# Kernel optimization log

Measured on AMD Instinct MI355X. Metric: run time of the kernel, lower is better.

Reference implementation:

```python
import jax, jax.numpy as jnp
import numpy as np

N_NODES = 100000
N_EDGES = 640000
NODE_D = 128   # node_emb_dim == edge_type_emb_dim (required by reverse-net input dim)
MSG_D = 128


def setup_inputs() -> dict:
    key = jax.random.key(0)
    ks = jax.random.split(key, 10)
    cat_d = 3 * NODE_D  # 2*node_emb + edge_type_emb
    s_msg = 1.0 / np.sqrt(cat_d)
    s_upd = 1.0 / np.sqrt(MSG_D)
    return {
        "node_features": jax.random.normal(ks[0], (N_NODES, NODE_D), jnp.float32),
        "edge_features": jax.random.normal(ks[1], (N_EDGES, NODE_D), jnp.float32),
        "from_idx": jax.random.randint(ks[2], (N_EDGES,), 0, N_NODES, jnp.int32),
        "to_idx": jax.random.randint(ks[3], (N_EDGES,), 0, N_NODES, jnp.int32),
        # message net (Linear + ReLU)
        "W_msg": jax.random.uniform(ks[4], (cat_d, MSG_D), jnp.float32, -s_msg, s_msg),
        "b_msg": jnp.zeros((MSG_D,), jnp.float32),
        # reverse message net (separate params)
        "W_rev": jax.random.uniform(ks[5], (cat_d, MSG_D), jnp.float32, -s_msg, s_msg),
        "b_rev": jnp.zeros((MSG_D,), jnp.float32),
        # node-update MLP (Linear + ReLU), residual update
        "W_upd": jax.random.uniform(ks[6], (MSG_D, NODE_D), jnp.float32, -s_upd, s_upd),
        "b_upd": jnp.zeros((NODE_D,), jnp.float32),
    }


def reference(node_features, edge_features, from_idx, to_idx,
              W_msg, b_msg, W_rev, b_rev, W_upd, b_upd):
    # gather endpoints and concat with edge features: [n_edges, 3*node_d]
    edge_inputs = jnp.concatenate(
        [node_features[from_idx], node_features[to_idx], edge_features], axis=-1)
    # forward + reverse message nets (same inputs, different params), summed
    messages = (jax.nn.relu(edge_inputs @ W_msg + b_msg)
                + jax.nn.relu(edge_inputs @ W_rev + b_rev))
    # scatter-sum into destination nodes: [n_nodes, msg_d]
    aggregated = jax.ops.segment_sum(messages, to_idx, num_segments=N_NODES)
    # residual node update: node + MLP(agg)
    return node_features + jax.nn.relu(aggregated @ W_upd + b_upd)
```

## Files before the change

kernel.cpp:

```cpp
#include <hip/hip_runtime.h>
#include <hip/hip_bf16.h>

#define N_NODES 100000
#define N_EDGES 640000

typedef __bf16 bf16_t;
typedef __bf16 bf16x8 __attribute__((ext_vector_type(8)));
typedef float f32x4 __attribute__((ext_vector_type(4)));
typedef float f4 __attribute__((ext_vector_type(4)));
typedef unsigned int u32x4 __attribute__((ext_vector_type(4)));

__device__ __forceinline__ float bflo(unsigned int u) { return __uint_as_float(u << 16); }
__device__ __forceinline__ float bfhi(unsigned int u) { return __uint_as_float(u & 0xffff0000u); }
__device__ __forceinline__ unsigned int bfpack(float a, float b) {
    union { bf16_t h[2]; unsigned int u; } pk;
    pk.h[0] = (bf16_t)a; pk.h[1] = (bf16_t)b;
    return pk.u;
}

__global__ void hist_kernel(const int* __restrict__ to_idx, int* __restrict__ hist) {
    int e = blockIdx.x * 256 + threadIdx.x;
    if (e < N_EDGES) atomicAdd(&hist[to_idx[e]], 1);
}

#define SCAN_CH 1000

__global__ __launch_bounds__(1024)
void scan_reduce_kernel(const int* __restrict__ hist, int* __restrict__ bsum) {
    __shared__ int red[1024];
    int b = blockIdx.x, t = threadIdx.x;
    int v = (t < SCAN_CH) ? hist[b * SCAN_CH + t] : 0;
    red[t] = v;
    __syncthreads();
    for (int off = 512; off > 0; off >>= 1) {
        if (t < off) red[t] += red[t + off];
        __syncthreads();
    }
    if (t == 0) bsum[b] = red[0];
}

__global__ __launch_bounds__(128)
void scan_base_kernel(const int* __restrict__ bsum, int* __restrict__ bbase) {
    __shared__ int s[128];
    int t = threadIdx.x;
    int v = (t < 100) ? bsum[t] : 0;
    s[t] = v;
    __syncthreads();
    for (int off = 1; off < 128; off <<= 1) {
        int u = (t >= off) ? s[t - off] : 0;
        __syncthreads();
        s[t] += u;
        __syncthreads();
    }
    if (t < 100) bbase[t] = s[t] - v;
}

__global__ __launch_bounds__(1024)
void scan_final_kernel(const int* __restrict__ hist,
                       const int* __restrict__ bbase,
                       int* __restrict__ cursor,
                       int* __restrict__ row_start) {
    __shared__ int s[1024];
    int b = blockIdx.x, t = threadIdx.x;
    int v = (t < SCAN_CH) ? hist[b * SCAN_CH + t] : 0;
    s[t] = v;
    __syncthreads();
    for (int off = 1; off < 1024; off <<= 1) {
        int u = (t >= off) ? s[t - off] : 0;
        __syncthreads();
        s[t] += u;
        __syncthreads();
    }
    int excl = bbase[b] + s[t] - v;
    if (t < SCAN_CH) {
        cursor[b * SCAN_CH + t] = excl;
        row_start[b * SCAN_CH + t] = excl;
    }
    if (b == 99 && t == SCAN_CH - 1) row_start[N_NODES] = excl + v;
}

__global__ void inv_scatter_kernel(const int* __restrict__ to_idx,
                                   int* __restrict__ cursor,
                                   int* __restrict__ inv) {
    int e = blockIdx.x * 256 + threadIdx.x;
    if (e < N_EDGES) {
        int pos = atomicAdd(&cursor[to_idx[e]], 1);
        inv[e] = pos;
    }
}

__global__ void prep_w_new(const float* __restrict__ Wmsg,
                           const float* __restrict__ Wrev,
                           const float* __restrict__ Wupd,
                           bf16_t* __restrict__ Wt1,
                           bf16_t* __restrict__ WtE,
                           bf16_t* __restrict__ WtU) {
    int idx = blockIdx.x * 256 + threadIdx.x;
    if (idx < 512 * 128) {
        int p = idx >> 7, k = idx & 127;
        int blk = p >> 7, c = p & 127;
        float v;
        if (blk == 0)      v = Wmsg[k * 128 + c];
        else if (blk == 1) v = Wrev[k * 128 + c];
        else if (blk == 2) v = Wmsg[(128 + k) * 128 + c];
        else               v = Wrev[(128 + k) * 128 + c];
        Wt1[idx] = (bf16_t)v;
    }
    if (idx < 256 * 128) {
        int p = idx >> 7, k = idx & 127;
        float v = (p < 128) ? Wmsg[(256 + k) * 128 + p]
                            : Wrev[(256 + k) * 128 + (p - 128)];
        WtE[idx] = (bf16_t)v;
    }
    if (idx < 128 * 128) {
        int n = idx >> 7, p = idx & 127;
        int colp = 32 * (p >> 5) + ((p >> 1) & 15) + 16 * (p & 1);
        WtU[idx] = (bf16_t)Wupd[colp * 128 + n];
    }
}

__global__ __launch_bounds__(512, 4)
void proj_node_kernel(const float* __restrict__ nodef,
                      const bf16_t* __restrict__ Wt1,
                      unsigned int* __restrict__ A_u) {
    __shared__ char lds_raw[64 * 256];
    const int tid = threadIdx.x;
    const int nb = blockIdx.x * 64;
    const int by = blockIdx.y;

#pragma unroll
    for (int j = 0; j < 4; ++j) {
        int linear = tid + 512 * j;
        int r = linear >> 5, q = linear & 31;
        int node = nb + r;
        f4 v = (f4){0.f, 0.f, 0.f, 0.f};
        if (node < N_NODES)
            v = *reinterpret_cast<const f4*>(nodef + (size_t)node * 128 + q * 4);
        union { bf16_t b[4]; uint2 u; } pk;
        pk.b[0] = (bf16_t)v[0]; pk.b[1] = (bf16_t)v[1];
        pk.b[2] = (bf16_t)v[2]; pk.b[3] = (bf16_t)v[3];
        int byte = (r * 256 + q * 8) ^ ((r & 7) << 4);
        *reinterpret_cast<uint2*>(lds_raw + byte) = pk.u;
    }
    __syncthreads();

    const int wv = tid >> 6;
    const int wr = wv >> 2, wc = wv & 3;
    const int lane = tid & 63;
    const int lhi = lane >> 4, llo = lane & 15;

    f32x4 acc[2][4];
#pragma unroll
    for (int m = 0; m < 2; ++m)
#pragma unroll
        for (int n = 0; n < 4; ++n)
            acc[m][n] = (f32x4){0.f, 0.f, 0.f, 0.f};

    const bf16_t* bptr[4];
#pragma unroll
    for (int n = 0; n < 4; ++n) {
        int colb = (n < 2) ? (wc * 32 + 16 * n) : (128 + wc * 32 + 16 * (n - 2));
        bptr[n] = Wt1 + (size_t)(by * 256 + colb + llo) * 128 + lhi * 8;
    }

#pragma unroll
    for (int k0 = 0; k0 < 4; ++k0) {
        bf16x8 a[2], b[4];
#pragma unroll
        for (int m = 0; m < 2; ++m) {
            int ra = wr * 32 + 16 * m + llo;
            int byte = (ra * 256 + (k0 * 32 + lhi * 8) * 2) ^ ((ra & 7) << 4);
            a[m] = *reinterpret_cast<const bf16x8*>(lds_raw + byte);
        }
#pragma unroll
        for (int n = 0; n < 4; ++n)
            b[n] = *reinterpret_cast<const bf16x8*>(bptr[n] + k0 * 32);
#pragma unroll
        for (int m = 0; m < 2; ++m)
#pragma unroll
            for (int n = 0; n < 4; ++n)
                acc[m][n] = __builtin_amdgcn_mfma_f32_16x16x32_bf16(a[m], b[n], acc[m][n], 0, 0, 0);
    }

    const int wli = wc * 16 + llo;
#pragma unroll
    for (int m = 0; m < 2; ++m) {
        int rbase = wr * 32 + 16 * m + lhi * 4;
#pragma unroll
        for (int r = 0; r < 4; ++r) {
            int node = nb + rbase + r;
            if (node < N_NODES) {
                size_t base = (size_t)node * 256 + by * 128;
                uint2 pr;
                pr.x = bfpack(acc[m][0][r], acc[m][1][r]);
                pr.y = bfpack(acc[m][2][r], acc[m][3][r]);
                *reinterpret_cast<uint2*>(A_u + base + 2 * wli) = pr;
            }
        }
    }
}

__global__ __launch_bounds__(256, 4)
void edge_fused_kernel(const float* __restrict__ edgef,
                       const int* __restrict__ from_idx,
                       const int* __restrict__ to_idx,
                       const int* __restrict__ inv,
                       const unsigned int* __restrict__ A_u,
                       const bf16_t* __restrict__ WtE,
                       const float* __restrict__ b_msg,
                       const float* __restrict__ b_rev,
                       unsigned int* __restrict__ msgs_u) {
    __shared__ char lds_raw[32 * 256];
    __shared__ int s_from[32], s_dst[32], s_inv[32];

    const int tid = threadIdx.x;
    const int eb = blockIdx.x * 32;

    if (tid < 32) {
        s_from[tid] = from_idx[eb + tid];
        s_dst[tid]  = to_idx[eb + tid];
        s_inv[tid]  = inv[eb + tid];
    }

#pragma unroll
    for (int j = 0; j < 4; ++j) {
        int linear = tid + 256 * j;
        int r = linear >> 5, q = linear & 31;
        f4 v = *reinterpret_cast<const f4*>(edgef + (size_t)(eb + r) * 128 + q * 4);
        union { bf16_t b[4]; uint2 u; } pk;
        pk.b[0] = (bf16_t)v[0]; pk.b[1] = (bf16_t)v[1];
        pk.b[2] = (bf16_t)v[2]; pk.b[3] = (bf16_t)v[3];
        int byte = (r * 256 + q * 8) ^ ((r & 7) << 4);
        *reinterpret_cast<uint2*>(lds_raw + byte) = pk.u;
    }
    __syncthreads();

    const int wc = tid >> 6;
    const int lane = tid & 63;
    const int lhi = lane >> 4, llo = lane & 15;
    const int wli = wc * 16 + llo;

    uint2 gF[2][4], gT[2][4];
#pragma unroll
    for (int m = 0; m < 2; ++m) {
#pragma unroll
        for (int r = 0; r < 4; ++r) {
            int rr = 16 * m + lhi * 4 + r;
            gF[m][r] = *reinterpret_cast<const uint2*>(
                A_u + (size_t)s_from[rr] * 256 + 2 * wli);
            gT[m][r] = *reinterpret_cast<const uint2*>(
                A_u + (size_t)s_dst[rr] * 256 + 128 + 2 * wli);
        }
    }

    f32x4 acc[2][4];
#pragma unroll
    for (int m = 0; m < 2; ++m)
#pragma unroll
        for (int n = 0; n < 4; ++n)
            acc[m][n] = (f32x4){0.f, 0.f, 0.f, 0.f};

    const bf16_t* bptr[4];
#pragma unroll
    for (int n = 0; n < 4; ++n) {
        int colb = (n < 2) ? (wc * 32 + 16 * n) : (128 + wc * 32 + 16 * (n - 2));
        bptr[n] = WtE + (size_t)(colb + llo) * 128 + lhi * 8;
    }

#pragma unroll
    for (int k0 = 0; k0 < 4; ++k0) {
        bf16x8 a[2], b[4];
#pragma unroll
        for (int m = 0; m < 2; ++m) {
            int ra = 16 * m + llo;
            int byte = (ra * 256 + (k0 * 32 + lhi * 8) * 2) ^ ((ra & 7) << 4);
            a[m] = *reinterpret_cast<const bf16x8*>(lds_raw + byte);
        }
#pragma unroll
        for (int n = 0; n < 4; ++n)
            b[n] = *reinterpret_cast<const bf16x8*>(bptr[n] + k0 * 32);
#pragma unroll
        for (int m = 0; m < 2; ++m)
#pragma unroll
            for (int n = 0; n < 4; ++n)
                acc[m][n] = __builtin_amdgcn_mfma_f32_16x16x32_bf16(a[m], b[n], acc[m][n], 0, 0, 0);
    }

    const int c0 = wc * 32 + llo;
    const float bm0 = b_msg[c0], bm1 = b_msg[c0 + 16];
    const float br0 = b_rev[c0], br1 = b_rev[c0 + 16];
#pragma unroll
    for (int m = 0; m < 2; ++m) {
#pragma unroll
        for (int r = 0; r < 4; ++r) {
            int rr = 16 * m + lhi * 4 + r;
            float m0 = fmaxf(acc[m][0][r] + bm0 + bflo(gF[m][r].x) + bflo(gT[m][r].x), 0.f);
            float m1 = fmaxf(acc[m][1][r] + bm1 + bfhi(gF[m][r].x) + bfhi(gT[m][r].x), 0.f);
            float r0 = fmaxf(acc[m][2][r] + br0 + bflo(gF[m][r].y) + bflo(gT[m][r].y), 0.f);
            float r1 = fmaxf(acc[m][3][r] + br1 + bfhi(gF[m][r].y) + bfhi(gT[m][r].y), 0.f);
            msgs_u[(size_t)s_inv[rr] * 64 + wli] = bfpack(m0 + r0, m1 + r1);
        }
    }
}

__global__ __launch_bounds__(256, 4)
void node_upd_kernel(const unsigned int* __restrict__ msgs_u,
                     const int* __restrict__ row_start,
                     const float* __restrict__ nodef,
                     const bf16_t* __restrict__ WtU,
                     const float* __restrict__ b_upd,
                     float* __restrict__ out) {
    __shared__ char lds_raw[64 * 256];
    __shared__ int s_rs[65];

    const int tid = threadIdx.x;
    const int nb = blockIdx.x * 64;

    if (tid < 65) {
        int nid = nb + tid;
        s_rs[tid] = (nid <= N_NODES) ? row_start[nid] : N_EDGES;
    }
    __syncthreads();

    {
        const int r = tid >> 2;
        const int q = tid & 3;
        float s[32];
#pragma unroll
        for (int i = 0; i < 32; ++i) s[i] = 0.f;
        const int rs = s_rs[r], re = s_rs[r + 1];
        int e = rs;
        for (; e + 1 < re; e += 2) {
            const u32x4* p0 = reinterpret_cast<const u32x4*>(msgs_u + (size_t)e * 64 + q * 16);
            const u32x4* p1 = reinterpret_cast<const u32x4*>(msgs_u + (size_t)(e + 1) * 64 + q * 16);
            u32x4 w0[4], w1[4];
#pragma unroll
            for (int i = 0; i < 4; ++i) { w0[i] = p0[i]; w1[i] = p1[i]; }
#pragma unroll
            for (int i = 0; i < 4; ++i) {
                s[8*i+0] += bflo(w0[i][0]) + bflo(w1[i][0]);
                s[8*i+1] += bfhi(w0[i][0]) + bfhi(w1[i][0]);
                s[8*i+2] += bflo(w0[i][1]) + bflo(w1[i][1]);
                s[8*i+3] += bfhi(w0[i][1]) + bfhi(w1[i][1]);
                s[8*i+4] += bflo(w0[i][2]) + bflo(w1[i][2]);
                s[8*i+5] += bfhi(w0[i][2]) + bfhi(w1[i][2]);
                s[8*i+6] += bflo(w0[i][3]) + bflo(w1[i][3]);
                s[8*i+7] += bfhi(w0[i][3]) + bfhi(w1[i][3]);
            }
        }
        if (e < re) {
            const u32x4* p = reinterpret_cast<const u32x4*>(msgs_u + (size_t)e * 64 + q * 16);
#pragma unroll
            for (int i = 0; i < 4; ++i) {
                u32x4 w = p[i];
                s[8*i+0] += bflo(w[0]); s[8*i+1] += bfhi(w[0]);
                s[8*i+2] += bflo(w[1]); s[8*i+3] += bfhi(w[1]);
                s[8*i+4] += bflo(w[2]); s[8*i+5] += bfhi(w[2]);
                s[8*i+6] += bflo(w[3]); s[8*i+7] += bfhi(w[3]);
            }
        }
#pragma unroll
        for (int i = 0; i < 4; ++i) {
            union { bf16_t b[8]; u32x4 u; } pk;
#pragma unroll
            for (int w = 0; w < 8; ++w) pk.b[w] = (bf16_t)s[8*i + w];
            int byte = (r * 256 + q * 64 + i * 16) ^ ((r & 7) << 4);
            *reinterpret_cast<u32x4*>(lds_raw + byte) = pk.u;
        }
    }
    __syncthreads();

    const int wv = tid >> 6;
    const int lane = tid & 63;
    const int lhi = lane >> 4, llo = lane & 15;

    f32x4 acc[4][2];
#pragma unroll
    for (int m = 0; m < 4; ++m)
#pragma unroll
        for (int n = 0; n < 2; ++n)
            acc[m][n] = (f32x4){0.f, 0.f, 0.f, 0.f};

#pragma unroll
    for (int k0 = 0; k0 < 4; ++k0) {
        bf16x8 a[4], b[2];
#pragma unroll
        for (int m = 0; m < 4; ++m) {
            int ra = 16 * m + llo;
            int byte = (ra * 256 + (k0 * 32 + lhi * 8) * 2) ^ ((ra & 7) << 4);
            a[m] = *reinterpret_cast<const bf16x8*>(lds_raw + byte);
        }
#pragma unroll
        for (int n = 0; n < 2; ++n) {
            int col = wv * 32 + 16 * n + llo;
            b[n] = *reinterpret_cast<const bf16x8*>(WtU + (size_t)col * 128 + k0 * 32 + lhi * 8);
        }
#pragma unroll
        for (int m = 0; m < 4; ++m)
#pragma unroll
            for (int n = 0; n < 2; ++n)
                acc[m][n] = __builtin_amdgcn_mfma_f32_16x16x32_bf16(a[m], b[n], acc[m][n], 0, 0, 0);
    }

#pragma unroll
    for (int m = 0; m < 4; ++m) {
        int rbase = 16 * m + lhi * 4;
#pragma unroll
        for (int r = 0; r < 4; ++r) {
            int i = nb + rbase + r;
            if (i < N_NODES) {
#pragma unroll
                for (int n = 0; n < 2; ++n) {
                    int c = wv * 32 + 16 * n + llo;
                    out[(size_t)i * 128 + c] =
                        nodef[(size_t)i * 128 + c]
                        + fmaxf(acc[m][n][r] + b_upd[c], 0.f);
                }
            }
        }
    }
}

__global__ __launch_bounds__(256)
void convert_nodef_kernel(const float* __restrict__ nodef,
                          unsigned short* __restrict__ nodef_bf) {
    int i = blockIdx.x * 256 + threadIdx.x;
    if (i < N_NODES * 32) {
        f4 v = *reinterpret_cast<const f4*>(nodef + (size_t)i * 4);
        union { bf16_t b[4]; unsigned long long ll; } pk;
        pk.b[0] = (bf16_t)v[0]; pk.b[1] = (bf16_t)v[1];
        pk.b[2] = (bf16_t)v[2]; pk.b[3] = (bf16_t)v[3];
        *reinterpret_cast<unsigned long long*>(nodef_bf + (size_t)i * 4) = pk.ll;
    }
}

__global__ void prep_w_old(const float* __restrict__ Wmsg,
                           const float* __restrict__ Wrev,
                           const float* __restrict__ Wupd,
                           bf16_t* __restrict__ WtAB,
                           bf16_t* __restrict__ WtU) {
    int idx = blockIdx.x * 256 + threadIdx.x;
    if (idx < 256 * 384) {
        int n = idx / 384;
        int k = idx - n * 384;
        float v = (n < 128) ? Wmsg[k * 128 + n] : Wrev[k * 128 + (n - 128)];
        WtAB[idx] = (bf16_t)v;
    }
    if (idx < 128 * 128) {
        int n = idx >> 7, p = idx & 127;
        int colp = 32 * (p >> 5) + ((p >> 1) & 15) + 16 * (p & 1);
        WtU[idx] = (bf16_t)Wupd[colp * 128 + n];
    }
}

__global__ __launch_bounds__(512, 4)
void edge_msg_old_kernel(const unsigned short* __restrict__ nodef_bf,
                         const float* __restrict__ edgef,
                         const int* __restrict__ from_idx,
                         const int* __restrict__ to_idx,
                         const int* __restrict__ inv,
                         const bf16_t* __restrict__ WtAB,
                         const float* __restrict__ b_msg,
                         const float* __restrict__ b_rev,
                         unsigned int* __restrict__ msgs_u) {
    __shared__ char lds_raw[64 * 384];
    __shared__ int s_from[64], s_dst[64], s_inv[64];

    const int tid = threadIdx.x;
    const int eb = blockIdx.x * 64;

    if (tid < 64) {
        s_from[tid] = from_idx[eb + tid];
        s_dst[tid]  = to_idx[eb + tid];
        s_inv[tid]  = inv[eb + tid];
    }

    const int wv = tid >> 6;
    const int wr = wv >> 2, wc = wv & 3;
    const int lane = tid & 63;
    const int lhi = lane >> 4, llo = lane & 15;

    f32x4 acc[2][4];
#pragma unroll
    for (int m = 0; m < 2; ++m)
#pragma unroll
        for (int n = 0; n < 4; ++n)
            acc[m][n] = (f32x4){0.f, 0.f, 0.f, 0.f};

    const bf16_t* bptr[4];
#pragma unroll
    for (int n = 0; n < 4; ++n) {
        int colb = (n < 2) ? (wc * 32 + 16 * n) : (128 + wc * 32 + 16 * (n - 2));
        bptr[n] = WtAB + (size_t)(colb + llo) * 384 + lhi * 8;
    }

    __syncthreads();

#pragma unroll
    for (int j = 0; j < 3; ++j) {
        int linear = tid + 512 * j;
        int r = linear / 24;
        int q = linear - r * 24;
        const u32x4* src = (q < 16)
            ? reinterpret_cast<const u32x4*>(nodef_bf + (size_t)s_from[r] * 128) + q
            : reinterpret_cast<const u32x4*>(nodef_bf + (size_t)s_dst[r] * 128) + (q - 16);
        u32x4 v = *src;
        int byte = (r * 384 + q * 16) ^ ((r & 7) << 4);
        *reinterpret_cast<u32x4*>(lds_raw + byte) = v;
    }
    __syncthreads();

#pragma unroll
    for (int k0 = 0; k0 < 6; ++k0) {
        bf16x8 a[2], b[4];
#pragma unroll
        for (int m = 0; m < 2; ++m) {
            int ra = wr * 32 + 16 * m + llo;
            int byte = (ra * 384 + k0 * 64 + lhi * 16) ^ ((ra & 7) << 4);
            a[m] = *reinterpret_cast<const bf16x8*>(lds_raw + byte);
        }
#pragma unroll
        for (int n = 0; n < 4; ++n)
            b[n] = *reinterpret_cast<const bf16x8*>(bptr[n] + k0 * 32);
#pragma unroll
        for (int m = 0; m < 2; ++m)
#pragma unroll
            for (int n = 0; n < 4; ++n)
                acc[m][n] = __builtin_amdgcn_mfma_f32_16x16x32_bf16(a[m], b[n], acc[m][n], 0, 0, 0);
    }
    __syncthreads();

#pragma unroll
    for (int j = 0; j < 3; ++j) {
        int linear = tid + 512 * j;
        int r = linear / 24;
        int qq = linear - r * 24;
        u32x4 w;
        if (qq < 8) {
            w = *(reinterpret_cast<const u32x4*>(nodef_bf + (size_t)s_dst[r] * 128) + 8 + qq);
        } else {
            int c = qq - 8;
            const f4* ep = reinterpret_cast<const f4*>(edgef + (size_t)(eb + r) * 128 + c * 8);
            f4 v0 = ep[0];
            f4 v1 = ep[1];
            union { bf16_t b[8]; u32x4 u; } pk;
            pk.b[0] = (bf16_t)v0[0]; pk.b[1] = (bf16_t)v0[1];
            pk.b[2] = (bf16_t)v0[2]; pk.b[3] = (bf16_t)v0[3];
            pk.b[4] = (bf16_t)v1[0]; pk.b[5] = (bf16_t)v1[1];
            pk.b[6] = (bf16_t)v1[2]; pk.b[7] = (bf16_t)v1[3];
            w = pk.u;
        }
        int byte = (r * 384 + qq * 16) ^ ((r & 7) << 4);
        *reinterpret_cast<u32x4*>(lds_raw + byte) = w;
    }
    __syncthreads();

#pragma unroll
    for (int k0 = 0; k0 < 6; ++k0) {
        bf16x8 a[2], b[4];
#pragma unroll
        for (int m = 0; m < 2; ++m) {
            int ra = wr * 32 + 16 * m + llo;
            int byte = (ra * 384 + k0 * 64 + lhi * 16) ^ ((ra & 7) << 4);
            a[m] = *reinterpret_cast<const bf16x8*>(lds_raw + byte);
        }
#pragma unroll
        for (int n = 0; n < 4; ++n)
            b[n] = *reinterpret_cast<const bf16x8*>(bptr[n] + (6 + k0) * 32);
#pragma unroll
        for (int m = 0; m < 2; ++m)
#pragma unroll
            for (int n = 0; n < 4; ++n)
                acc[m][n] = __builtin_amdgcn_mfma_f32_16x16x32_bf16(a[m], b[n], acc[m][n], 0, 0, 0);
    }

    const int c0 = wc * 32 + llo;
    const float bm0 = b_msg[c0], br0 = b_rev[c0];
    const float bm1 = b_msg[c0 + 16], br1 = b_rev[c0 + 16];
#pragma unroll
    for (int m = 0; m < 2; ++m) {
        int rbase = wr * 32 + 16 * m + lhi * 4;
#pragma unroll
        for (int r = 0; r < 4; ++r) {
            float v0 = fmaxf(acc[m][0][r] + bm0, 0.f) + fmaxf(acc[m][2][r] + br0, 0.f);
            float v1 = fmaxf(acc[m][1][r] + bm1, 0.f) + fmaxf(acc[m][3][r] + br1, 0.f);
            msgs_u[(size_t)s_inv[rbase + r] * 64 + wc * 16 + llo] = bfpack(v0, v1);
        }
    }
}

extern "C" void kernel_launch(void* const* d_in, const int* in_sizes, int n_in,
                              void* d_out, int out_size, void* d_ws, size_t ws_size,
                              hipStream_t stream) {
    const float* nodef    = (const float*)d_in[0];
    const float* edgef    = (const float*)d_in[1];
    const int*   from_idx = (const int*)d_in[2];
    const int*   to_idx   = (const int*)d_in[3];
    const float* Wmsg     = (const float*)d_in[4];
    const float* bmsg     = (const float*)d_in[5];
    const float* Wrev     = (const float*)d_in[6];
    const float* brev     = (const float*)d_in[7];
    const float* Wupd     = (const float*)d_in[8];
    const float* bupd     = (const float*)d_in[9];
    float* out = (float*)d_out;
    char* ws = (char*)d_ws;

    if (ws_size >= 271000000) {
        unsigned int* A_u      = (unsigned int*)ws;
        unsigned int* msgs_u   = (unsigned int*)(ws + 102400000);
        bf16_t*       Wt1      = (bf16_t*)(ws + 266240000);
        bf16_t*       WtE      = (bf16_t*)(ws + 266371072);
        bf16_t*       WtU      = (bf16_t*)(ws + 266436608);
        int*          hist     = (int*)(ws + 266469376);
        int*          cursor   = (int*)(ws + 266869376);
        int*          rowstart = (int*)(ws + 267269376);
        int*          inv      = (int*)(ws + 267669392);
        int*          bsum     = (int*)(ws + 270229392);
        int*          bbase    = (int*)(ws + 270229792);

        hipMemsetAsync(hist, 0, (size_t)N_NODES * sizeof(int), stream);
        prep_w_new<<<256, 256, 0, stream>>>(Wmsg, Wrev, Wupd, Wt1, WtE, WtU);
        hist_kernel<<<(N_EDGES + 255) / 256, 256, 0, stream>>>(to_idx, hist);
        scan_reduce_kernel<<<100, 1024, 0, stream>>>(hist, bsum);
        scan_base_kernel<<<1, 128, 0, stream>>>(bsum, bbase);
        scan_final_kernel<<<100, 1024, 0, stream>>>(hist, bbase, cursor, rowstart);
        inv_scatter_kernel<<<(N_EDGES + 255) / 256, 256, 0, stream>>>(to_idx, cursor, inv);
        proj_node_kernel<<<dim3((N_NODES + 63) / 64, 2), 512, 0, stream>>>(nodef, Wt1, A_u);
        edge_fused_kernel<<<N_EDGES / 32, 256, 0, stream>>>(
            edgef, from_idx, to_idx, inv, A_u, WtE, bmsg, brev, msgs_u);
        node_upd_kernel<<<(N_NODES + 63) / 64, 256, 0, stream>>>(
            msgs_u, rowstart, nodef, WtU, bupd, out);
    } else {
        unsigned int*   msgs_u   = (unsigned int*)ws;
        bf16_t*         WtAB     = (bf16_t*)(ws + 163840000);
        bf16_t*         WtU      = (bf16_t*)(ws + 164036608);
        unsigned short* nodef_bf = (unsigned short*)(ws + 164069376);
        int*            hist     = (int*)(ws + 189669376);
        int*            cursor   = (int*)(ws + 190069376);
        int*            rowstart = (int*)(ws + 190469376);
        int*            inv      = (int*)(ws + 190869392);
        int*            bsum     = (int*)(ws + 193429392);
        int*            bbase    = (int*)(ws + 193429792);

        hipMemsetAsync(hist, 0, (size_t)N_NODES * sizeof(int), stream);
        convert_nodef_kernel<<<12500, 256, 0, stream>>>(nodef, nodef_bf);
        prep_w_old<<<384, 256, 0, stream>>>(Wmsg, Wrev, Wupd, WtAB, WtU);
        hist_kernel<<<(N_EDGES + 255) / 256, 256, 0, stream>>>(to_idx, hist);
        scan_reduce_kernel<<<100, 1024, 0, stream>>>(hist, bsum);
        scan_base_kernel<<<1, 128, 0, stream>>>(bsum, bbase);
        scan_final_kernel<<<100, 1024, 0, stream>>>(hist, bbase, cursor, rowstart);
        inv_scatter_kernel<<<(N_EDGES + 255) / 256, 256, 0, stream>>>(to_idx, cursor, inv);
        edge_msg_old_kernel<<<N_EDGES / 64, 512, 0, stream>>>(
            nodef_bf, edgef, from_idx, to_idx, inv, WtAB, bmsg, brev, msgs_u);
        node_upd_kernel<<<(N_NODES + 63) / 64, 256, 0, stream>>>(
            msgs_u, rowstart, nodef, WtU, bupd, out);
    }
}
```

Baseline: 457.8 us.

## Process four edge tiles per block with double-buffered LDS staging in edge kernel

The edge kernel now handles 128 edges per block as four 32-edge tiles. Each tile's edge features are prefetched into registers and written to a second LDS buffer while the current tile's MFMAs run, so global loads overlap compute. The launch count drops by a factor of four, which also amortises the per-block index and bias setup. The small-workspace fallback path and its old kernels are removed, so the code now assumes a large enough workspace, and the extra live registers may reduce occupancy.

```diff
diff --git a/kernel.cpp b/kernel.cpp
--- a/kernel.cpp
+++ b/kernel.cpp
@@ -210,56 +210,23 @@
                        const float* __restrict__ b_msg,
                        const float* __restrict__ b_rev,
                        unsigned int* __restrict__ msgs_u) {
-    __shared__ char lds_raw[32 * 256];
-    __shared__ int s_from[32], s_dst[32], s_inv[32];
+    __shared__ char lds_raw[2][8192];
+    __shared__ int s_from[128], s_dst[128], s_inv[128];
 
     const int tid = threadIdx.x;
-    const int eb = blockIdx.x * 32;
-
-    if (tid < 32) {
-        s_from[tid] = from_idx[eb + tid];
-        s_dst[tid]  = to_idx[eb + tid];
-        s_inv[tid]  = inv[eb + tid];
-    }
-
-#pragma unroll
-    for (int j = 0; j < 4; ++j) {
-        int linear = tid + 256 * j;
-        int r = linear >> 5, q = linear & 31;
-        f4 v = *reinterpret_cast<const f4*>(edgef + (size_t)(eb + r) * 128 + q * 4);
-        union { bf16_t b[4]; uint2 u; } pk;
-        pk.b[0] = (bf16_t)v[0]; pk.b[1] = (bf16_t)v[1];
-        pk.b[2] = (bf16_t)v[2]; pk.b[3] = (bf16_t)v[3];
-        int byte = (r * 256 + q * 8) ^ ((r & 7) << 4);
-        *reinterpret_cast<uint2*>(lds_raw + byte) = pk.u;
-    }
-    __syncthreads();
+    const size_t eb0 = (size_t)blockIdx.x * 128;
+
+    if (tid < 128) {
+        s_from[tid] = from_idx[eb0 + tid];
+        s_dst[tid]  = to_idx[eb0 + tid];
+        s_inv[tid]  = inv[eb0 + tid];
+    }
 
     const int wc = tid >> 6;
     const int lane = tid & 63;
     const int lhi = lane >> 4, llo = lane & 15;
     const int wli = wc * 16 + llo;
 
-    uint2 gF[2][4], gT[2][4];
-#pragma unroll
-    for (int m = 0; m < 2; ++m) {
-#pragma unroll
-        for (int r = 0; r < 4; ++r) {
-            int rr = 16 * m + lhi * 4 + r;
-            gF[m][r] = *reinterpret_cast<const uint2*>(
-                A_u + (size_t)s_from[rr] * 256 + 2 * wli);
-            gT[m][r] = *reinterpret_cast<const uint2*>(
-                A_u + (size_t)s_dst[rr] * 256 + 128 + 2 * wli);
-        }
-    }
-
-    f32x4 acc[2][4];
-#pragma unroll
-    for (int m = 0; m < 2; ++m)
-#pragma unroll
-        for (int n = 0; n < 4; ++n)
-            acc[m][n] = (f32x4){0.f, 0.f, 0.f, 0.f};
-
     const bf16_t* bptr[4];
 #pragma unroll
     for (int n = 0; n < 4; ++n) {
@@ -267,39 +234,128 @@
         bptr[n] = WtE + (size_t)(colb + llo) * 128 + lhi * 8;
     }
 
-#pragma unroll
-    for (int k0 = 0; k0 < 4; ++k0) {
-        bf16x8 a[2], b[4];
-#pragma unroll
-        for (int m = 0; m < 2; ++m) {
-            int ra = 16 * m + llo;
-            int byte = (ra * 256 + (k0 * 32 + lhi * 8) * 2) ^ ((ra & 7) << 4);
-            a[m] = *reinterpret_cast<const bf16x8*>(lds_raw + byte);
-        }
-#pragma unroll
-        for (int n = 0; n < 4; ++n)
-            b[n] = *reinterpret_cast<const bf16x8*>(bptr[n] + k0 * 32);
-#pragma unroll
-        for (int m = 0; m < 2; ++m)
-#pragma unroll
-            for (int n = 0; n < 4; ++n)
-                acc[m][n] = __builtin_amdgcn_mfma_f32_16x16x32_bf16(a[m], b[n], acc[m][n], 0, 0, 0);
-    }
-
     const int c0 = wc * 32 + llo;
     const float bm0 = b_msg[c0], bm1 = b_msg[c0 + 16];
     const float br0 = b_rev[c0], br1 = b_rev[c0 + 16];
-#pragma unroll
-    for (int m = 0; m < 2; ++m) {
-#pragma unroll
-        for (int r = 0; r < 4; ++r) {
-            int rr = 16 * m + lhi * 4 + r;
-            float m0 = fmaxf(acc[m][0][r] + bm0 + bflo(gF[m][r].x) + bflo(gT[m][r].x), 0.f);
-            float m1 = fmaxf(acc[m][1][r] + bm1 + bfhi(gF[m][r].x) + bfhi(gT[m][r].x), 0.f);
-            float r0 = fmaxf(acc[m][2][r] + br0 + bflo(gF[m][r].y) + bflo(gT[m][r].y), 0.f);
-            float r1 = fmaxf(acc[m][3][r] + br1 + bfhi(gF[m][r].y) + bfhi(gT[m][r].y), 0.f);
-            msgs_u[(size_t)s_inv[rr] * 64 + wli] = bfpack(m0 + r0, m1 + r1);
-        }
+
+    f4 st[4];
+#pragma unroll
+    for (int j = 0; j < 4; ++j) {
+        int lin = tid + 256 * j, r = lin >> 5, q = lin & 31;
+        st[j] = *reinterpret_cast<const f4*>(edgef + (eb0 + r) * 128 + q * 4);
+    }
+#pragma unroll
+    for (int j = 0; j < 4; ++j) {
+        int lin = tid + 256 * j, r = lin >> 5, q = lin & 31;
+        union { bf16_t b[4]; uint2 u; } pk;
+        pk.b[0] = (bf16_t)st[j][0]; pk.b[1] = (bf16_t)st[j][1];
+        pk.b[2] = (bf16_t)st[j][2]; pk.b[3] = (bf16_t)st[j][3];
+        int byte = (r * 256 + q * 8) ^ ((r & 7) << 4);
+        *reinterpret_cast<uint2*>(&lds_raw[0][0] + byte) = pk.u;
+    }
+    __syncthreads();
+
+#pragma unroll
+    for (int t = 0; t < 4; ++t) {
+        const int cur = t & 1;
+
+        bf16x8 bA[2][4];
+#pragma unroll
+        for (int k0 = 0; k0 < 2; ++k0)
+#pragma unroll
+            for (int n = 0; n < 4; ++n)
+                bA[k0][n] = *reinterpret_cast<const bf16x8*>(bptr[n] + k0 * 32);
+
+        uint2 gF[2][4], gT[2][4];
+#pragma unroll
+        for (int m = 0; m < 2; ++m)
+#pragma unroll
+            for (int r = 0; r < 4; ++r) {
+                int rr = t * 32 + 16 * m + lhi * 4 + r;
+                gF[m][r] = *reinterpret_cast<const uint2*>(
+                    A_u + (size_t)s_from[rr] * 256 + 2 * wli);
+                gT[m][r] = *reinterpret_cast<const uint2*>(
+                    A_u + (size_t)s_dst[rr] * 256 + 128 + 2 * wli);
+            }
+
+        if (t < 3) {
+#pragma unroll
+            for (int j = 0; j < 4; ++j) {
+                int lin = tid + 256 * j, r = lin >> 5, q = lin & 31;
+                st[j] = *reinterpret_cast<const f4*>(
+                    edgef + (eb0 + (size_t)(t + 1) * 32 + r) * 128 + q * 4);
+            }
+        }
+
+        f32x4 acc[2][4];
+#pragma unroll
+        for (int m = 0; m < 2; ++m)
+#pragma unroll
+            for (int n = 0; n < 4; ++n)
+                acc[m][n] = (f32x4){0.f, 0.f, 0.f, 0.f};
+#pragma unroll
+        for (int k0 = 0; k0 < 2; ++k0) {
+            bf16x8 a[2];
+#pragma unroll
+            for (int m = 0; m < 2; ++m) {
+                int ra = 16 * m + llo;
+                int byte = (ra * 256 + (k0 * 32 + lhi * 8) * 2) ^ ((ra & 7) << 4);
+                a[m] = *reinterpret_cast<const bf16x8*>(&lds_raw[cur][0] + byte);
+            }
+#pragma unroll
+            for (int m = 0; m < 2; ++m)
+#pragma unroll
+                for (int n = 0; n < 4; ++n)
+                    acc[m][n] = __builtin_amdgcn_mfma_f32_16x16x32_bf16(a[m], bA[k0][n], acc[m][n], 0, 0, 0);
+        }
+
+#pragma unroll
+        for (int k0 = 0; k0 < 2; ++k0)
+#pragma unroll
+            for (int n = 0; n < 4; ++n)
+                bA[k0][n] = *reinterpret_cast<const bf16x8*>(bptr[n] + (2 + k0) * 32);
+
+#pragma unroll
+        for (int k0 = 0; k0 < 2; ++k0) {
+            bf16x8 a[2];
+#pragma unroll
+            for (int m = 0; m < 2; ++m) {
+                int ra = 16 * m + llo;
+                int byte = (ra * 256 + ((2 + k0) * 32 + lhi * 8) * 2) ^ ((ra & 7) << 4);
+                a[m] = *reinterpret_cast<const bf16x8*>(&lds_raw[cur][0] + byte);
+            }
+#pragma unroll
+            for (int m = 0; m < 2; ++m)
+#pragma unroll
+                for (int n = 0; n < 4; ++n)
+                    acc[m][n] = __builtin_amdgcn_mfma_f32_16x16x32_bf16(a[m], bA[k0][n], acc[m][n], 0, 0, 0);
+        }
+
+        if (t < 3) {
+#pragma unroll
+            for (int j = 0; j < 4; ++j) {
+                int lin = tid + 256 * j, r = lin >> 5, q = lin & 31;
+                union { bf16_t b[4]; uint2 u; } pk;
+                pk.b[0] = (bf16_t)st[j][0]; pk.b[1] = (bf16_t)st[j][1];
+                pk.b[2] = (bf16_t)st[j][2]; pk.b[3] = (bf16_t)st[j][3];
+                int byte = (r * 256 + q * 8) ^ ((r & 7) << 4);
+                *reinterpret_cast<uint2*>(&lds_raw[cur ^ 1][0] + byte) = pk.u;
+            }
+        }
+
+#pragma unroll
+        for (int m = 0; m < 2; ++m)
+#pragma unroll
+            for (int r = 0; r < 4; ++r) {
+                int rr = t * 32 + 16 * m + lhi * 4 + r;
+                float m0 = fmaxf(acc[m][0][r] + bm0 + bflo(gF[m][r].x) + bflo(gT[m][r].x), 0.f);
+                float m1 = fmaxf(acc[m][1][r] + bm1 + bfhi(gF[m][r].x) + bfhi(gT[m][r].x), 0.f);
+                float r0 = fmaxf(acc[m][2][r] + br0 + bflo(gF[m][r].y) + bflo(gT[m][r].y), 0.f);
+                float r1 = fmaxf(acc[m][3][r] + br1 + bfhi(gF[m][r].y) + bfhi(gT[m][r].y), 0.f);
+                msgs_u[(size_t)s_inv[rr] * 64 + wli] = bfpack(m0 + r0, m1 + r1);
+            }
+
+        __syncthreads();
     }
 }
 
@@ -417,174 +473,6 @@
                         + fmaxf(acc[m][n][r] + b_upd[c], 0.f);
                 }
             }
-        }
-    }
-}
-
-__global__ __launch_bounds__(256)
-void convert_nodef_kernel(const float* __restrict__ nodef,
-                          unsigned short* __restrict__ nodef_bf) {
-    int i = blockIdx.x * 256 + threadIdx.x;
-    if (i < N_NODES * 32) {
-        f4 v = *reinterpret_cast<const f4*>(nodef + (size_t)i * 4);
-        union { bf16_t b[4]; unsigned long long ll; } pk;
-        pk.b[0] = (bf16_t)v[0]; pk.b[1] = (bf16_t)v[1];
-        pk.b[2] = (bf16_t)v[2]; pk.b[3] = (bf16_t)v[3];
-        *reinterpret_cast<unsigned long long*>(nodef_bf + (size_t)i * 4) = pk.ll;
-    }
-}
-
-__global__ void prep_w_old(const float* __restrict__ Wmsg,
-                           const float* __restrict__ Wrev,
-                           const float* __restrict__ Wupd,
-                           bf16_t* __restrict__ WtAB,
-                           bf16_t* __restrict__ WtU) {
-    int idx = blockIdx.x * 256 + threadIdx.x;
-    if (idx < 256 * 384) {
-        int n = idx / 384;
-        int k = idx - n * 384;
-        float v = (n < 128) ? Wmsg[k * 128 + n] : Wrev[k * 128 + (n - 128)];
-        WtAB[idx] = (bf16_t)v;
-    }
-    if (idx < 128 * 128) {
-        int n = idx >> 7, p = idx & 127;
-        int colp = 32 * (p >> 5) + ((p >> 1) & 15) + 16 * (p & 1);
-        WtU[idx] = (bf16_t)Wupd[colp * 128 + n];
-    }
-}
-
-__global__ __launch_bounds__(512, 4)
-void edge_msg_old_kernel(const unsigned short* __restrict__ nodef_bf,
-                         const float* __restrict__ edgef,
-                         const int* __restrict__ from_idx,
-                         const int* __restrict__ to_idx,
-                         const int* __restrict__ inv,
-                         const bf16_t* __restrict__ WtAB,
-                         const float* __restrict__ b_msg,
-                         const float* __restrict__ b_rev,
-                         unsigned int* __restrict__ msgs_u) {
-    __shared__ char lds_raw[64 * 384];
-    __shared__ int s_from[64], s_dst[64], s_inv[64];
-
-    const int tid = threadIdx.x;
-    const int eb = blockIdx.x * 64;
-
-    if (tid < 64) {
-        s_from[tid] = from_idx[eb + tid];
-        s_dst[tid]  = to_idx[eb + tid];
-        s_inv[tid]  = inv[eb + tid];
-    }
-
-    const int wv = tid >> 6;
-    const int wr = wv >> 2, wc = wv & 3;
-    const int lane = tid & 63;
-    const int lhi = lane >> 4, llo = lane & 15;
-
-    f32x4 acc[2][4];
-#pragma unroll
-    for (int m = 0; m < 2; ++m)
-#pragma unroll
-        for (int n = 0; n < 4; ++n)
-            acc[m][n] = (f32x4){0.f, 0.f, 0.f, 0.f};
-
-    const bf16_t* bptr[4];
-#pragma unroll
-    for (int n = 0; n < 4; ++n) {
-        int colb = (n < 2) ? (wc * 32 + 16 * n) : (128 + wc * 32 + 16 * (n - 2));
-        bptr[n] = WtAB + (size_t)(colb + llo) * 384 + lhi * 8;
-    }
-
-    __syncthreads();
-
-#pragma unroll
-    for (int j = 0; j < 3; ++j) {
-        int linear = tid + 512 * j;
-        int r = linear / 24;
-        int q = linear - r * 24;
-        const u32x4* src = (q < 16)
-            ? reinterpret_cast<const u32x4*>(nodef_bf + (size_t)s_from[r] * 128) + q
-            : reinterpret_cast<const u32x4*>(nodef_bf + (size_t)s_dst[r] * 128) + (q - 16);
-        u32x4 v = *src;
-        int byte = (r * 384 + q * 16) ^ ((r & 7) << 4);
-        *reinterpret_cast<u32x4*>(lds_raw + byte) = v;
-    }
-    __syncthreads();
-
-#pragma unroll
-    for (int k0 = 0; k0 < 6; ++k0) {
-        bf16x8 a[2], b[4];
-#pragma unroll
-        for (int m = 0; m < 2; ++m) {
-            int ra = wr * 32 + 16 * m + llo;
-            int byte = (ra * 384 + k0 * 64 + lhi * 16) ^ ((ra & 7) << 4);
-            a[m] = *reinterpret_cast<const bf16x8*>(lds_raw + byte);
-        }
-#pragma unroll
-        for (int n = 0; n < 4; ++n)
-            b[n] = *reinterpret_cast<const bf16x8*>(bptr[n] + k0 * 32);
-#pragma unroll
-        for (int m = 0; m < 2; ++m)
-#pragma unroll
-            for (int n = 0; n < 4; ++n)
-                acc[m][n] = __builtin_amdgcn_mfma_f32_16x16x32_bf16(a[m], b[n], acc[m][n], 0, 0, 0);
-    }
-    __syncthreads();
-
-#pragma unroll
-    for (int j = 0; j < 3; ++j) {
-        int linear = tid + 512 * j;
-        int r = linear / 24;
-        int qq = linear - r * 24;
-        u32x4 w;
-        if (qq < 8) {
-            w = *(reinterpret_cast<const u32x4*>(nodef_bf + (size_t)s_dst[r] * 128) + 8 + qq);
-        } else {
-            int c = qq - 8;
-            const f4* ep = reinterpret_cast<const f4*>(edgef + (size_t)(eb + r) * 128 + c * 8);
-            f4 v0 = ep[0];
-            f4 v1 = ep[1];
-            union { bf16_t b[8]; u32x4 u; } pk;
-            pk.b[0] = (bf16_t)v0[0]; pk.b[1] = (bf16_t)v0[1];
-            pk.b[2] = (bf16_t)v0[2]; pk.b[3] = (bf16_t)v0[3];
-            pk.b[4] = (bf16_t)v1[0]; pk.b[5] = (bf16_t)v1[1];
-            pk.b[6] = (bf16_t)v1[2]; pk.b[7] = (bf16_t)v1[3];
-            w = pk.u;
-        }
-        int byte = (r * 384 + qq * 16) ^ ((r & 7) << 4);
-        *reinterpret_cast<u32x4*>(lds_raw + byte) = w;
-    }
-    __syncthreads();
-
-#pragma unroll
-    for (int k0 = 0; k0 < 6; ++k0) {
-        bf16x8 a[2], b[4];
-#pragma unroll
-        for (int m = 0; m < 2; ++m) {
-            int ra = wr * 32 + 16 * m + llo;
-            int byte = (ra * 384 + k0 * 64 + lhi * 16) ^ ((ra & 7) << 4);
-            a[m] = *reinterpret_cast<const bf16x8*>(lds_raw + byte);
-        }
-#pragma unroll
-        for (int n = 0; n < 4; ++n)
-            b[n] = *reinterpret_cast<const bf16x8*>(bptr[n] + (6 + k0) * 32);
-#pragma unroll
-        for (int m = 0; m < 2; ++m)
-#pragma unroll
-            for (int n = 0; n < 4; ++n)
-                acc[m][n] = __builtin_amdgcn_mfma_f32_16x16x32_bf16(a[m], b[n], acc[m][n], 0, 0, 0);
-    }
-
-    const int c0 = wc * 32 + llo;
-    const float bm0 = b_msg[c0], br0 = b_rev[c0];
-    const float bm1 = b_msg[c0 + 16], br1 = b_rev[c0 + 16];
-#pragma unroll
-    for (int m = 0; m < 2; ++m) {
-        int rbase = wr * 32 + 16 * m + lhi * 4;
-#pragma unroll
-        for (int r = 0; r < 4; ++r) {
-            float v0 = fmaxf(acc[m][0][r] + bm0, 0.f) + fmaxf(acc[m][2][r] + br0, 0.f);
-            float v1 = fmaxf(acc[m][1][r] + bm1, 0.f) + fmaxf(acc[m][3][r] + br1, 0.f);
-            msgs_u[(size_t)s_inv[rbase + r] * 64 + wc * 16 + llo] = bfpack(v0, v1);
         }
     }
 }
@@ -605,54 +493,28 @@
     float* out = (float*)d_out;
     char* ws = (char*)d_ws;
 
-    if (ws_size >= 271000000) {
-        unsigned int* A_u      = (unsigned int*)ws;
-        unsigned int* msgs_u   = (unsigned int*)(ws + 102400000);
-        bf16_t*       Wt1      = (bf16_t*)(ws + 266240000);
-        bf16_t*       WtE      = (bf16_t*)(ws + 266371072);
-        bf16_t*       WtU      = (bf16_t*)(ws + 266436608);
-        int*          hist     = (int*)(ws + 266469376);
-        int*          cursor   = (int*)(ws + 266869376);
-        int*          rowstart = (int*)(ws + 267269376);
-        int*          inv      = (int*)(ws + 267669392);
-        int*          bsum     = (int*)(ws + 270229392);
-        int*          bbase    = (int*)(ws + 270229792);
-
-        hipMemsetAsync(hist, 0, (size_t)N_NODES * sizeof(int), stream);
-        prep_w_new<<<256, 256, 0, stream>>>(Wmsg, Wrev, Wupd, Wt1, WtE, WtU);
-        hist_kernel<<<(N_EDGES + 255) / 256, 256, 0, stream>>>(to_idx, hist);
-        scan_reduce_kernel<<<100, 1024, 0, stream>>>(hist, bsum);
-        scan_base_kernel<<<1, 128, 0, stream>>>(bsum, bbase);
-        scan_final_kernel<<<100, 1024, 0, stream>>>(hist, bbase, cursor, rowstart);
-        inv_scatter_kernel<<<(N_EDGES + 255) / 256, 256, 0, stream>>>(to_idx, cursor, inv);
-        proj_node_kernel<<<dim3((N_NODES + 63) / 64, 2), 512, 0, stream>>>(nodef, Wt1, A_u);
-        edge_fused_kernel<<<N_EDGES / 32, 256, 0, stream>>>(
-            edgef, from_idx, to_idx, inv, A_u, WtE, bmsg, brev, msgs_u);
-        node_upd_kernel<<<(N_NODES + 63) / 64, 256, 0, stream>>>(
-            msgs_u, rowstart, nodef, WtU, bupd, out);
-    } else {
-        unsigned int*   msgs_u   = (unsigned int*)ws;
-        bf16_t*         WtAB     = (bf16_t*)(ws + 163840000);
-        bf16_t*         WtU      = (bf16_t*)(ws + 164036608);
-        unsigned short* nodef_bf = (unsigned short*)(ws + 164069376);
-        int*            hist     = (int*)(ws + 189669376);
-        int*            cursor   = (int*)(ws + 190069376);
-        int*            rowstart = (int*)(ws + 190469376);
-        int*            inv      = (int*)(ws + 190869392);
-        int*            bsum     = (int*)(ws + 193429392);
-        int*            bbase    = (int*)(ws + 193429792);
-
-        hipMemsetAsync(hist, 0, (size_t)N_NODES * sizeof(int), stream);
-        convert_nodef_kernel<<<12500, 256, 0, stream>>>(nodef, nodef_bf);
-        prep_w_old<<<384, 256, 0, stream>>>(Wmsg, Wrev, Wupd, WtAB, WtU);
-        hist_kernel<<<(N_EDGES + 255) / 256, 256, 0, stream>>>(to_idx, hist);
-        scan_reduce_kernel<<<100, 1024, 0, stream>>>(hist, bsum);
-        scan_base_kernel<<<1, 128, 0, stream>>>(bsum, bbase);
-        scan_final_kernel<<<100, 1024, 0, stream>>>(hist, bbase, cursor, rowstart);
-        inv_scatter_kernel<<<(N_EDGES + 255) / 256, 256, 0, stream>>>(to_idx, cursor, inv);
-        edge_msg_old_kernel<<<N_EDGES / 64, 512, 0, stream>>>(
-            nodef_bf, edgef, from_idx, to_idx, inv, WtAB, bmsg, brev, msgs_u);
-        node_upd_kernel<<<(N_NODES + 63) / 64, 256, 0, stream>>>(
-            msgs_u, rowstart, nodef, WtU, bupd, out);
-    }
-}
+    unsigned int* A_u      = (unsigned int*)ws;
+    unsigned int* msgs_u   = (unsigned int*)(ws + 102400000);
+    bf16_t*       Wt1      = (bf16_t*)(ws + 266240000);
+    bf16_t*       WtE      = (bf16_t*)(ws + 266371072);
+    bf16_t*       WtU      = (bf16_t*)(ws + 266436608);
+    int*          hist     = (int*)(ws + 266469376);
+    int*          cursor   = (int*)(ws + 266869376);
+    int*          rowstart = (int*)(ws + 267269376);
+    int*          inv      = (int*)(ws + 267669392);
+    int*          bsum     = (int*)(ws + 270229392);
+    int*          bbase    = (int*)(ws + 270229792);
+
+    hipMemsetAsync(hist, 0, (size_t)N_NODES * sizeof(int), stream);
+    prep_w_new<<<256, 256, 0, stream>>>(Wmsg, Wrev, Wupd, Wt1, WtE, WtU);
+    hist_kernel<<<(N_EDGES + 255) / 256, 256, 0, stream>>>(to_idx, hist);
+    scan_reduce_kernel<<<100, 1024, 0, stream>>>(hist, bsum);
+    scan_base_kernel<<<1, 128, 0, stream>>>(bsum, bbase);
+    scan_final_kernel<<<100, 1024, 0, stream>>>(hist, bbase, cursor, rowstart);
+    inv_scatter_kernel<<<(N_EDGES + 255) / 256, 256, 0, stream>>>(to_idx, cursor, inv);
+    proj_node_kernel<<<dim3((N_NODES + 63) / 64, 2), 512, 0, stream>>>(nodef, Wt1, A_u);
+    edge_fused_kernel<<<N_EDGES / 128, 256, 0, stream>>>(
+        edgef, from_idx, to_idx, inv, A_u, WtE, bmsg, brev, msgs_u);
+    node_upd_kernel<<<(N_NODES + 63) / 64, 256, 0, stream>>>(
+        msgs_u, rowstart, nodef, WtU, bupd, out);
+}
```

After: 457.5 us. About the same (-0.1%).
